# Kernel tuning notes

Measured on AMD Instinct MI355X. Metric: run time of the kernel, lower is better.

The kernel has to match this reference:

```python
import jax, jax.numpy as jnp
import numpy as np

N_HOPS = 2
N_ENTITIES = 100000
EMB = 64
N_REL = 32
N_EDGES = 1000000


def _l2norm(x, eps=1e-12):
    # torch F.normalize: x / max(||x||_2, eps) per row
    n = jnp.sqrt(jnp.sum(x * x, axis=1, keepdims=True))
    return x / jnp.maximum(n, eps)


def setup_inputs() -> dict:
    key = jax.random.key(0)
    k1, k2, k3, k4, k5, k6 = jax.random.split(key, 6)
    return {
        "entity_emb": jax.random.normal(k1, (N_ENTITIES, EMB), dtype=jnp.float32),
        "edge_emb": jax.random.normal(k2, (N_REL, EMB), dtype=jnp.float32) * 0.1,
        "q_w": jax.random.normal(k3, (EMB, EMB), dtype=jnp.float32) * (1.0 / np.sqrt(EMB)),
        "k_w": jax.random.normal(k4, (EMB, EMB), dtype=jnp.float32) * (1.0 / np.sqrt(EMB)),
        "edge_index": jax.random.randint(k5, (2, N_EDGES), 0, N_ENTITIES, dtype=jnp.int32),
        "edge_type": jax.random.randint(k6, (N_EDGES,), 0, N_REL, dtype=jnp.int32),
        "mess_dropout": 0,
    }


def reference(entity_emb, edge_emb, q_w, k_w, edge_index, edge_type, mess_dropout):
    head = edge_index[0]
    tail = edge_index[1]
    rel = edge_emb[edge_type]                      # [E, D]
    kg = jnp.zeros_like(entity_emb)
    agg = entity_emb
    for _ in range(N_HOPS):
        # edge-wise tanh attention score
        left = (agg @ q_w)[head]                   # [E, D] (factor GEMM out of gather)
        right = jnp.tanh((rel * agg[tail]) @ k_w)  # [E, D]
        att = jnp.sum(left * right, axis=1)        # [E]
        # scatter_softmax over head segments
        m = jax.ops.segment_max(att, head, num_segments=N_ENTITIES)
        e = jnp.exp(att - jax.lax.stop_gradient(m)[head])
        denom = jax.ops.segment_sum(e, head, num_segments=N_ENTITIES)
        w = e / denom[head]                        # [E]
        # weighted messages + scatter_mean aggregation
        msg = w[:, None] * rel * agg[tail]         # [E, D]
        s = jax.ops.segment_sum(msg, head, num_segments=N_ENTITIES)
        cnt = jax.ops.segment_sum(jnp.ones_like(w), head, num_segments=N_ENTITIES)
        agg = s / jnp.maximum(cnt, 1.0)[:, None]
        # mess_dropout=False path; normalize + residual accumulation
        agg = _l2norm(agg)
        kg = kg + agg + entity_emb
    return kg
```

## Files before the change

kernel.cpp:

```cpp
#include <hip/hip_runtime.h>
#include <math.h>

#define EMB 64
#define MAXREL 32
#define BSHIFT 9
#define BCAP 6912
#define CH 2048

typedef short bf16x8 __attribute__((ext_vector_type(8)));
typedef float f32x4 __attribute__((ext_vector_type(4)));

__device__ __forceinline__ short f2bf(float f) {
    unsigned u = __float_as_uint(f);
    u += 0x7FFFu + ((u >> 16) & 1u);
    return (short)(u >> 16);
}

#if __has_builtin(__builtin_amdgcn_cvt_pk_bf16_f32)
__device__ __forceinline__ short2 cvt2(float a, float b) {
    return __builtin_bit_cast(short2, __builtin_amdgcn_cvt_pk_bf16_f32(a, b));
}
#else
__device__ __forceinline__ short2 cvt2(float a, float b) {
    return make_short2(f2bf(a), f2bf(b));
}
#endif

__device__ __forceinline__ float lo_bf(unsigned d) { return __uint_as_float(d << 16); }
__device__ __forceinline__ float hi_bf(unsigned d) { return __uint_as_float(d & 0xffff0000u); }
__device__ __forceinline__ float bfs(short s) {
    return __uint_as_float(((unsigned)(unsigned short)s) << 16);
}

__device__ __forceinline__ bf16x8 pack8bf(uint4 U, float4 r0, float4 r1) {
    short2 c0 = cvt2(lo_bf(U.x) * r0.x, hi_bf(U.x) * r0.y);
    short2 c1 = cvt2(lo_bf(U.y) * r0.z, hi_bf(U.y) * r0.w);
    short2 c2 = cvt2(lo_bf(U.z) * r1.x, hi_bf(U.z) * r1.y);
    short2 c3 = cvt2(lo_bf(U.w) * r1.z, hi_bf(U.w) * r1.w);
    bf16x8 a;
    a[0] = c0.x; a[1] = c0.y; a[2] = c1.x; a[3] = c1.y;
    a[4] = c2.x; a[5] = c2.y; a[6] = c3.x; a[7] = c3.y;
    return a;
}

__device__ __forceinline__ float fast_rcp(float x) {
#if __has_builtin(__builtin_amdgcn_rcpf)
    return __builtin_amdgcn_rcpf(x);
#else
    return 1.0f / x;
#endif
}

__device__ __forceinline__ float fast_tanh(float x) {
    float ax = fabsf(x);
    float z = __expf(2.0f * ax);
    float r = 1.0f - 2.0f * fast_rcp(z + 1.0f);
    return copysignf(r, x);
}

__global__ void init_kernel(short4* __restrict__ aggbf, float4* __restrict__ kg,
                            const float4* __restrict__ ent, int n4) {
    int i = blockIdx.x * blockDim.x + threadIdx.x;
    if (i < n4) {
        float4 v = ent[i];
        short2 c0 = cvt2(v.x, v.y), c1 = cvt2(v.z, v.w);
        aggbf[i] = make_short4(c0.x, c0.y, c1.x, c1.y);
        kg[i] = make_float4(0.f, 0.f, 0.f, 0.f);
    }
}


__global__ void hist_kernel(int* __restrict__ deg, const int* __restrict__ head, int E) {
    int e = blockIdx.x * blockDim.x + threadIdx.x;
    if (e < E) atomicAdd(&deg[head[e]], 1);
}

__global__ void scan_blocks(const int* __restrict__ deg, int* __restrict__ excl,
                            int* __restrict__ bsum, int n) {
    __shared__ int wsum[4];
    int base = blockIdx.x * 1024;
    int t = threadIdx.x;
    int lane = t & 63, wid = t >> 6;
    int idx = base + t * 4;
    int v0 = (idx + 0 < n) ? deg[idx + 0] : 0;
    int v1 = (idx + 1 < n) ? deg[idx + 1] : 0;
    int v2 = (idx + 2 < n) ? deg[idx + 2] : 0;
    int v3 = (idx + 3 < n) ? deg[idx + 3] : 0;
    int s0 = v0, s1 = s0 + v1, s2 = s1 + v2, s3 = s2 + v3;
    int tsum = s3;
    int inc = tsum;
#pragma unroll
    for (int o = 1; o < 64; o <<= 1) { int u = __shfl_up(inc, o, 64); if (lane >= o) inc += u; }
    if (lane == 63) wsum[wid] = inc;
    __syncthreads();
    int woff = 0;
#pragma unroll
    for (int w = 0; w < 4; ++w) if (w < wid) woff += wsum[w];
    int texcl = woff + inc - tsum;
    if (idx + 0 < n) excl[idx + 0] = texcl;
    if (idx + 1 < n) excl[idx + 1] = texcl + s0;
    if (idx + 2 < n) excl[idx + 2] = texcl + s1;
    if (idx + 3 < n) excl[idx + 3] = texcl + s2;
    if (t == 255) bsum[blockIdx.x] = woff + inc;
}

__global__ void scan_sums(int* __restrict__ bsum, int* __restrict__ excl, int nb, int n, int E) {
    __shared__ int ws[4];
    int t = threadIdx.x;
    if (nb > 256) {
        if (t == 0) {
            int acc = 0;
            for (int b = 0; b < nb; ++b) { int v = bsum[b]; bsum[b] = acc; acc += v; }
            excl[n] = E;
        }
        return;
    }
    int lane = t & 63, wid = t >> 6;
    int v = (t < nb) ? bsum[t] : 0;
    int inc = v;
#pragma unroll
    for (int o = 1; o < 64; o <<= 1) { int u = __shfl_up(inc, o, 64); if (lane >= o) inc += u; }
    if (lane == 63) ws[wid] = inc;
    __syncthreads();
    int woff = 0;
#pragma unroll
    for (int w = 0; w < 4; ++w) if (w < wid) woff += ws[w];
    if (t < nb) bsum[t] = woff + inc - v;
    if (t == 0) excl[n] = E;
}

__global__ void scan_add(int* __restrict__ excl, const int* __restrict__ bsum, int n) {
    int i = blockIdx.x * blockDim.x + threadIdx.x;
    if (i < n) excl[i] += bsum[i >> 10];
}

__global__ void bucket_init(int* __restrict__ bcursor, const int* __restrict__ offsets,
                            int nb, int N) {
    int b = blockIdx.x * blockDim.x + threadIdx.x;
    if (b < nb) bcursor[b] = offsets[min(b << BSHIFT, N)];
}

__global__ void bucket_scatter(const int* __restrict__ head, const int* __restrict__ tail,
                               const int* __restrict__ etype, int* __restrict__ bcursor,
                               int2* __restrict__ tmp, int E, int nb) {
    __shared__ int lcnt[512];
    __shared__ int lbase[512];
    int t = threadIdx.x;
    int base = blockIdx.x * CH;
    for (int i = t; i < 512; i += 256) lcnt[i] = 0;
    __syncthreads();
    int myh[8];
#pragma unroll
    for (int i = 0; i < 8; ++i) {
        int e = base + i * 256 + t;
        if (e < E) {
            int h = head[e];
            myh[i] = h;
            atomicAdd(&lcnt[h >> BSHIFT], 1);
        } else myh[i] = -1;
    }
    __syncthreads();
    for (int b = t; b < nb; b += 256) {
        int c = lcnt[b];
        lbase[b] = (c > 0) ? atomicAdd(&bcursor[b], c) : 0;
        lcnt[b] = 0;
    }
    __syncthreads();
#pragma unroll
    for (int i = 0; i < 8; ++i) {
        int e = base + i * 256 + t;
        if (e < E) {
            int h = myh[i];
            int b = h >> BSHIFT;
            int pos = lbase[b] + atomicAdd(&lcnt[b], 1);
            tmp[pos] = make_int2(h, tail[e] | (etype[e] << 20));
        }
    }
}

__global__ void bucket_sort(const int* __restrict__ offsets, const int2* __restrict__ tmp,
                            int2* __restrict__ spair, int N) {
    __shared__ int2 staged[BCAP];
    __shared__ int lcur[1 << BSHIFT];
    int b = blockIdx.x;
    int h0 = b << BSHIFT;
    int h1 = min(h0 + (1 << BSHIFT), N);
    int r0 = offsets[h0], r1 = offsets[h1];
    int cnt = r1 - r0;
    int t = threadIdx.x;
    for (int h = h0 + t; h < h1; h += blockDim.x) lcur[h - h0] = offsets[h] - r0;
    __syncthreads();
    if (cnt <= BCAP) {
        for (int i = t; i < cnt; i += blockDim.x) {
            int2 rec = tmp[r0 + i];
            int lp = atomicAdd(&lcur[rec.x - h0], 1);
            staged[lp] = rec;
        }
        __syncthreads();
        for (int i = t; i < cnt; i += blockDim.x) spair[r0 + i] = staged[i];
    } else {
        for (int i = t; i < cnt; i += blockDim.x) {
            int2 rec = tmp[r0 + i];
            int lp = atomicAdd(&lcur[rec.x - h0], 1);
            spair[r0 + lp] = rec;
        }
    }
}


__device__ __forceinline__ void build_bfrags(bf16x8 bfrag[2][4], const float* __restrict__ W,
                                             int lane) {
    int koff = (lane >> 4) * 8;
    int n = lane & 15;
#pragma unroll
    for (int kh = 0; kh < 2; ++kh)
#pragma unroll
        for (int nt = 0; nt < 4; ++nt) {
            bf16x8 b;
#pragma unroll
            for (int j = 0; j < 8; ++j)
                b[j] = f2bf(W[(kh * 32 + koff + j) * EMB + nt * 16 + n]);
            bfrag[kh][nt] = b;
        }
}

__global__ void qproj_mfma_kernel(short* __restrict__ Qbf, const short* __restrict__ aggbf,
                                  const float* __restrict__ qw, int N) {
    int lane = threadIdx.x & 63;
    int gwave = blockIdx.x * (blockDim.x >> 6) + (threadIdx.x >> 6);
    int nwaves = gridDim.x * (blockDim.x >> 6);
    int row = lane & 15;
    int g = lane >> 4;
    int koff = g * 8;

    bf16x8 bfrag[2][4];
    build_bfrags(bfrag, qw, lane);

    int ntiles = (N + 15) >> 4;
    for (int tile = gwave; tile < ntiles; tile += nwaves) {
        int rIdx = min(tile * 16 + row, N - 1);
        const short* rowp = aggbf + (size_t)rIdx * EMB;
        bf16x8 a0 = *(const bf16x8*)(rowp + koff);
        bf16x8 a1 = *(const bf16x8*)(rowp + 32 + koff);
#pragma unroll
        for (int nt = 0; nt < 4; ++nt) {
            f32x4 acc = {0.f, 0.f, 0.f, 0.f};
            acc = __builtin_amdgcn_mfma_f32_16x16x32_bf16(a0, bfrag[0][nt], acc, 0, 0, 0);
            acc = __builtin_amdgcn_mfma_f32_16x16x32_bf16(a1, bfrag[1][nt], acc, 0, 0, 0);
#pragma unroll
            for (int reg = 0; reg < 4; ++reg) {
                int n2 = tile * 16 + g * 4 + reg;
                if (n2 < N) Qbf[(size_t)n2 * EMB + nt * 16 + (lane & 15)] = f2bf(acc[reg]);
            }
        }
    }
}

__global__ void att_mfma_kernel(float* __restrict__ att,
                                const short* __restrict__ aggbf, const short* __restrict__ Qbf,
                                const float* __restrict__ eemb, const float* __restrict__ kw,
                                const int2* __restrict__ spair, int E) {
    int lane = threadIdx.x & 63;
    int gwave = blockIdx.x * (blockDim.x >> 6) + (threadIdx.x >> 6);
    int nwaves = gridDim.x * (blockDim.x >> 6);
    int row = lane & 15;
    int g = lane >> 4;

    bf16x8 bfrag[2][4];
    build_bfrags(bfrag, kw, lane);

    int ntiles = (E + 15) >> 4;
    for (int tile = gwave; tile < ntiles; tile += nwaves) {
        int eld = min(tile * 16 + row, E - 1);
        int2 pr = spair[eld];
        int h = pr.x;
        int t = pr.y & 0xFFFFF;
        unsigned r = ((unsigned)pr.y) >> 20;
        const uint4* rowa = (const uint4*)(aggbf + (size_t)t * EMB);
        const float4* rl4 = (const float4*)(eemb + (size_t)r * EMB);
        uint4 U0 = rowa[g];
        uint4 U1 = rowa[4 + g];
        float4 y0 = rl4[g * 2], y1 = rl4[g * 2 + 1];
        float4 y2 = rl4[8 + g * 2], y3 = rl4[8 + g * 2 + 1];
        bf16x8 a0 = pack8bf(U0, y0, y1);
        bf16x8 a1 = pack8bf(U1, y2, y3);

        float sums0 = 0.f, sums1 = 0.f, sums2 = 0.f, sums3 = 0.f;
#pragma unroll
        for (int nt = 0; nt < 4; ++nt) {
            f32x4 acc = {0.f, 0.f, 0.f, 0.f};
            acc = __builtin_amdgcn_mfma_f32_16x16x32_bf16(a0, bfrag[0][nt], acc, 0, 0, 0);
            acc = __builtin_amdgcn_mfma_f32_16x16x32_bf16(a1, bfrag[1][nt], acc, 0, 0, 0);
#pragma unroll
            for (int reg = 0; reg < 4; ++reg) {
                int row2 = g * 4 + reg;
                int h2 = __shfl(h, row2, 64);
                float q = bfs(Qbf[(size_t)h2 * EMB + nt * 16 + (lane & 15)]);
                float v = q * fast_tanh(acc[reg]);
                if (reg == 0) sums0 += v;
                else if (reg == 1) sums1 += v;
                else if (reg == 2) sums2 += v;
                else sums3 += v;
            }
        }
#pragma unroll
        for (int m = 1; m <= 8; m <<= 1) {
            sums0 += __shfl_xor(sums0, m, 64);
            sums1 += __shfl_xor(sums1, m, 64);
            sums2 += __shfl_xor(sums2, m, 64);
            sums3 += __shfl_xor(sums3, m, 64);
        }
#pragma unroll
        for (int reg = 0; reg < 4; ++reg) {
            int row2 = g * 4 + reg;
            int e2 = tile * 16 + row2;
            float v = (reg == 0) ? sums0 : (reg == 1) ? sums1 : (reg == 2) ? sums2 : sums3;
            if ((lane & 15) == reg && e2 < E) att[e2] = v;
        }
    }
}

__global__ void head_agg_kernel(short* __restrict__ aggNewBf, float* __restrict__ kg,
                                const float* __restrict__ att, const short* __restrict__ aggOldBf,
                                const float* __restrict__ eemb, const float* __restrict__ ent,
                                const int* __restrict__ offsets, const int2* __restrict__ spair,
                                int N, int R) {
    __shared__ float4 elds4[MAXREL * 16];

    int tid = threadIdx.x;
    int lane = tid & 63;
    int wid = tid >> 6;
    int RS = (R < MAXREL) ? R : MAXREL;
    for (int i = tid; i < RS * 16; i += blockDim.x) elds4[i] = ((const float4*)eemb)[i];
    __syncthreads();

    int sub = lane >> 4;
    int q = lane & 15;
    int h = (blockIdx.x * (blockDim.x >> 6) + wid) * 4 + sub;
    if (h >= N) return;
    int beg = offsets[h], end = offsets[h + 1];
    int deg = end - beg;

    float m = -3.4e38f;
    for (int e = beg + q; e < end; e += 16) m = fmaxf(m, att[e]);
#pragma unroll
    for (int o = 1; o <= 8; o <<= 1) m = fmaxf(m, __shfl_xor(m, o, 64));

    float4 acc4 = make_float4(0.f, 0.f, 0.f, 0.f);
    float ssum = 0.f;
    int qbase = lane & 48;
    for (int c = beg; c < end; c += 16) {
        int e = c + q;
        float ev = 0.f; int tr = 0;
        if (e < end) {
            ev = __expf(att[e] - m);
            tr = spair[e].y;
        }
        ssum += ev;
        int nc = min(16, end - c);
        auto body = [&](int j) {
            int src = qbase | j;
            float ej = __shfl(ev, src, 64);
            int trj = __shfl(tr, src, 64);
            int tj = trj & 0xFFFFF;
            unsigned rj = ((unsigned)trj) >> 20;
            float4 ew = (rj < (unsigned)RS) ? elds4[rj * 16 + q]
                                            : ((const float4*)eemb)[(size_t)rj * 16 + q];
            uint2 X = ((const uint2*)(aggOldBf + (size_t)tj * EMB))[q];
            acc4.x += ej * ew.x * lo_bf(X.x);
            acc4.y += ej * ew.y * hi_bf(X.x);
            acc4.z += ej * ew.z * lo_bf(X.y);
            acc4.w += ej * ew.w * hi_bf(X.y);
        };
        if (nc == 16) {
#pragma unroll 4
            for (int j = 0; j < 16; ++j) body(j);
        } else {
            for (int j = 0; j < nc; ++j) body(j);
        }
    }
#pragma unroll
    for (int o = 1; o <= 8; o <<= 1) ssum += __shfl_xor(ssum, o, 64);

    float scale = (deg > 0) ? 1.0f / (ssum * (float)deg) : 0.f;
    float4 v = make_float4(acc4.x * scale, acc4.y * scale, acc4.z * scale, acc4.w * scale);
    float ss = v.x * v.x + v.y * v.y + v.z * v.z + v.w * v.w;
#pragma unroll
    for (int o = 1; o <= 8; o <<= 1) ss += __shfl_xor(ss, o, 64);
    float rinv = 1.0f / fmaxf(sqrtf(ss), 1e-12f);
    v.x *= rinv; v.y *= rinv; v.z *= rinv; v.w *= rinv;

    short2 c0 = cvt2(v.x, v.y), c1 = cvt2(v.z, v.w);
    ((short4*)aggNewBf)[(size_t)h * 16 + q] = make_short4(c0.x, c0.y, c1.x, c1.y);
    float4 kgv = ((float4*)kg)[(size_t)h * 16 + q];
    float4 ev2 = ((const float4*)ent)[(size_t)h * 16 + q];
    kgv.x += v.x + ev2.x; kgv.y += v.y + ev2.y;
    kgv.z += v.z + ev2.z; kgv.w += v.w + ev2.w;
    ((float4*)kg)[(size_t)h * 16 + q] = kgv;
}

extern "C" void kernel_launch(void* const* d_in, const int* in_sizes, int n_in,
                              void* d_out, int out_size, void* d_ws, size_t ws_size,
                              hipStream_t stream) {
    const float* ent  = (const float*)d_in[0];
    const float* eemb = (const float*)d_in[1];
    const float* qw   = (const float*)d_in[2];
    const float* kw   = (const float*)d_in[3];
    const int* eidx  = (const int*)d_in[4];
    const int* etype = (const int*)d_in[5];

    const int N = in_sizes[0] / EMB;
    const int R = in_sizes[1] / EMB;
    const int E = in_sizes[5];
    const int* head = eidx;
    const int* tail = eidx + E;

    float* kg = (float*)d_out;

    float* att   = (float*)d_ws;
    int2* spair  = (int2*)(att + E);
    int* offsets = (int*)(spair + E);
    int* deg     = offsets + (N + 1);
    int* bcursor = deg + N;
    int* bsum    = bcursor + N;
    uintptr_t pa = ((uintptr_t)(bsum + 1024) + 15) & ~(uintptr_t)15;
    short* aggbf_a = (short*)pa;
    short* aggbf_b = aggbf_a + (size_t)N * EMB;
    short* Qbf     = aggbf_b + (size_t)N * EMB;
    int2* tmp      = (int2*)Qbf;

    const int NT = 256;
    const int nb = (N + 1023) / 1024;
    const int nbk = (N + (1 << BSHIFT) - 1) >> BSHIFT;

    init_kernel<<<(N * EMB / 4 + NT - 1) / NT, NT, 0, stream>>>(
        (short4*)aggbf_a, (float4*)kg, (const float4*)ent, N * EMB / 4);
    hipMemsetAsync(deg, 0, (size_t)N * 4, stream);
    hist_kernel<<<(E + NT - 1) / NT, NT, 0, stream>>>(deg, head, E);
    scan_blocks<<<nb, NT, 0, stream>>>(deg, offsets, bsum, N);
    scan_sums<<<1, NT, 0, stream>>>(bsum, offsets, nb, N, E);
    scan_add<<<(N + NT - 1) / NT, NT, 0, stream>>>(offsets, bsum, N);
    bucket_init<<<(nbk + NT - 1) / NT, NT, 0, stream>>>(bcursor, offsets, nbk, N);
    bucket_scatter<<<(E + CH - 1) / CH, NT, 0, stream>>>(head, tail, etype, bcursor, tmp, E, nbk);
    bucket_sort<<<nbk, NT, 0, stream>>>(offsets, tmp, spair, N);

    short* curbf = aggbf_a;
    short* nxtbf = aggbf_b;
    for (int hop = 0; hop < 2; ++hop) {
        qproj_mfma_kernel<<<512, NT, 0, stream>>>(Qbf, curbf, qw, N);
        att_mfma_kernel<<<2048, NT, 0, stream>>>(att, curbf, Qbf, eemb, kw, spair, E);
        head_agg_kernel<<<(N + 15) / 16, NT, 0, stream>>>(nxtbf, kg, att, curbf,
                                                          eemb, ent, offsets, spair, N, R);
        short* ts = curbf; curbf = nxtbf; nxtbf = ts;
    }
}
```

Measured before the change: 420.0 us.

## Materialize per-edge rel*tail messages in att kernel and prefetch next tile

The attention kernel now writes each edge's bf16 rel*agg[tail] product (already computed as the MFMA A operand) to a workspace buffer in sorted-edge order. When the workspace is large enough, a new aggregation kernel reads those messages contiguously instead of gathering random tail rows and relation embeddings. The attention loop also software-prefetches the next tile's edge pair and tail rows and hoists the head-index shuffles. This trades 128 MB of extra writes and reads per hop for removing a random gather. The fallback path depends on workspace size, and the unroll factor is raised to 8.

```diff
diff --git a/kernel.cpp b/kernel.cpp
--- a/kernel.cpp
+++ b/kernel.cpp
@@ -42,6 +42,8 @@
     a[4] = c2.x; a[5] = c2.y; a[6] = c3.x; a[7] = c3.y;
     return a;
 }
+
+__device__ __forceinline__ uint4 asu4(bf16x8 v) { return __builtin_bit_cast(uint4, v); }
 
 __device__ __forceinline__ float fast_rcp(float x) {
 #if __has_builtin(__builtin_amdgcn_rcpf)
@@ -256,7 +258,7 @@
     }
 }
 
-__global__ void att_mfma_kernel(float* __restrict__ att,
+__global__ void att_mfma_kernel(float* __restrict__ att, short* __restrict__ Mout,
                                 const short* __restrict__ aggbf, const short* __restrict__ Qbf,
                                 const float* __restrict__ eemb, const float* __restrict__ kw,
                                 const int2* __restrict__ spair, int E) {
@@ -270,38 +272,63 @@
     build_bfrags(bfrag, kw, lane);
 
     int ntiles = (E + 15) >> 4;
-    for (int tile = gwave; tile < ntiles; tile += nwaves) {
-        int eld = min(tile * 16 + row, E - 1);
-        int2 pr = spair[eld];
+    int tile = gwave;
+    int2 pr = make_int2(0, 0);
+    uint4 U0 = make_uint4(0, 0, 0, 0), U1 = make_uint4(0, 0, 0, 0);
+    if (tile < ntiles) {
+        pr = spair[min(tile * 16 + row, E - 1)];
+        const uint4* rowa = (const uint4*)(aggbf + (size_t)(pr.y & 0xFFFFF) * EMB);
+        U0 = rowa[g];
+        U1 = rowa[4 + g];
+    }
+    for (; tile < ntiles; tile += nwaves) {
+        int tnext = tile + nwaves;
+        int2 prn = pr;
+        if (tnext < ntiles) prn = spair[min(tnext * 16 + row, E - 1)];
+
         int h = pr.x;
-        int t = pr.y & 0xFFFFF;
         unsigned r = ((unsigned)pr.y) >> 20;
-        const uint4* rowa = (const uint4*)(aggbf + (size_t)t * EMB);
         const float4* rl4 = (const float4*)(eemb + (size_t)r * EMB);
-        uint4 U0 = rowa[g];
-        uint4 U1 = rowa[4 + g];
         float4 y0 = rl4[g * 2], y1 = rl4[g * 2 + 1];
         float4 y2 = rl4[8 + g * 2], y3 = rl4[8 + g * 2 + 1];
         bf16x8 a0 = pack8bf(U0, y0, y1);
         bf16x8 a1 = pack8bf(U1, y2, y3);
 
+        uint4 U0n = U0, U1n = U1;
+        if (tnext < ntiles) {
+            const uint4* rowan = (const uint4*)(aggbf + (size_t)(prn.y & 0xFFFFF) * EMB);
+            U0n = rowan[g];
+            U1n = rowan[4 + g];
+        }
+
+        if (Mout) {
+            int e0 = tile * 16 + row;
+            if (e0 < E) {
+                uint4* mrow = (uint4*)(Mout + (size_t)e0 * EMB);
+                mrow[g] = asu4(a0);
+                mrow[4 + g] = asu4(a1);
+            }
+        }
+
+        int h2r0 = __shfl(h, g * 4 + 0, 64);
+        int h2r1 = __shfl(h, g * 4 + 1, 64);
+        int h2r2 = __shfl(h, g * 4 + 2, 64);
+        int h2r3 = __shfl(h, g * 4 + 3, 64);
+        const short* q0 = Qbf + (size_t)h2r0 * EMB + (lane & 15);
+        const short* q1 = Qbf + (size_t)h2r1 * EMB + (lane & 15);
+        const short* q2 = Qbf + (size_t)h2r2 * EMB + (lane & 15);
+        const short* q3 = Qbf + (size_t)h2r3 * EMB + (lane & 15);
+
         float sums0 = 0.f, sums1 = 0.f, sums2 = 0.f, sums3 = 0.f;
 #pragma unroll
         for (int nt = 0; nt < 4; ++nt) {
             f32x4 acc = {0.f, 0.f, 0.f, 0.f};
             acc = __builtin_amdgcn_mfma_f32_16x16x32_bf16(a0, bfrag[0][nt], acc, 0, 0, 0);
             acc = __builtin_amdgcn_mfma_f32_16x16x32_bf16(a1, bfrag[1][nt], acc, 0, 0, 0);
-#pragma unroll
-            for (int reg = 0; reg < 4; ++reg) {
-                int row2 = g * 4 + reg;
-                int h2 = __shfl(h, row2, 64);
-                float q = bfs(Qbf[(size_t)h2 * EMB + nt * 16 + (lane & 15)]);
-                float v = q * fast_tanh(acc[reg]);
-                if (reg == 0) sums0 += v;
-                else if (reg == 1) sums1 += v;
-                else if (reg == 2) sums2 += v;
-                else sums3 += v;
-            }
+            sums0 += bfs(q0[nt * 16]) * fast_tanh(acc[0]);
+            sums1 += bfs(q1[nt * 16]) * fast_tanh(acc[1]);
+            sums2 += bfs(q2[nt * 16]) * fast_tanh(acc[2]);
+            sums3 += bfs(q3[nt * 16]) * fast_tanh(acc[3]);
         }
 #pragma unroll
         for (int m = 1; m <= 8; m <<= 1) {
@@ -317,7 +344,71 @@
             float v = (reg == 0) ? sums0 : (reg == 1) ? sums1 : (reg == 2) ? sums2 : sums3;
             if ((lane & 15) == reg && e2 < E) att[e2] = v;
         }
-    }
+        pr = prn; U0 = U0n; U1 = U1n;
+    }
+}
+
+__global__ void head_agg_m_kernel(short* __restrict__ aggNewBf, float* __restrict__ kg,
+                                  const float* __restrict__ att, const short* __restrict__ M,
+                                  const float* __restrict__ ent, const int* __restrict__ offsets,
+                                  int N) {
+    int tid = threadIdx.x;
+    int lane = tid & 63;
+    int wid = tid >> 6;
+    int sub = lane >> 4;
+    int q = lane & 15;
+    int h = (blockIdx.x * (blockDim.x >> 6) + wid) * 4 + sub;
+    if (h >= N) return;
+    int beg = offsets[h], end = offsets[h + 1];
+    int deg = end - beg;
+
+    float m = -3.4e38f;
+    for (int e = beg + q; e < end; e += 16) m = fmaxf(m, att[e]);
+#pragma unroll
+    for (int o = 1; o <= 8; o <<= 1) m = fmaxf(m, __shfl_xor(m, o, 64));
+
+    float4 acc4 = make_float4(0.f, 0.f, 0.f, 0.f);
+    float ssum = 0.f;
+    int qbase = lane & 48;
+    for (int c = beg; c < end; c += 16) {
+        int e = c + q;
+        float ev = 0.f;
+        if (e < end) ev = __expf(att[e] - m);
+        ssum += ev;
+        int nc = min(16, end - c);
+        auto body = [&](int j) {
+            float ej = __shfl(ev, qbase | j, 64);
+            uint2 X = ((const uint2*)(M + (size_t)(c + j) * EMB))[q];
+            acc4.x += ej * lo_bf(X.x);
+            acc4.y += ej * hi_bf(X.x);
+            acc4.z += ej * lo_bf(X.y);
+            acc4.w += ej * hi_bf(X.y);
+        };
+        if (nc == 16) {
+#pragma unroll 8
+            for (int j = 0; j < 16; ++j) body(j);
+        } else {
+            for (int j = 0; j < nc; ++j) body(j);
+        }
+    }
+#pragma unroll
+    for (int o = 1; o <= 8; o <<= 1) ssum += __shfl_xor(ssum, o, 64);
+
+    float scale = (deg > 0) ? 1.0f / (ssum * (float)deg) : 0.f;
+    float4 v = make_float4(acc4.x * scale, acc4.y * scale, acc4.z * scale, acc4.w * scale);
+    float ss = v.x * v.x + v.y * v.y + v.z * v.z + v.w * v.w;
+#pragma unroll
+    for (int o = 1; o <= 8; o <<= 1) ss += __shfl_xor(ss, o, 64);
+    float rinv = 1.0f / fmaxf(sqrtf(ss), 1e-12f);
+    v.x *= rinv; v.y *= rinv; v.z *= rinv; v.w *= rinv;
+
+    short2 c0 = cvt2(v.x, v.y), c1 = cvt2(v.z, v.w);
+    ((short4*)aggNewBf)[(size_t)h * 16 + q] = make_short4(c0.x, c0.y, c1.x, c1.y);
+    float4 kgv = ((float4*)kg)[(size_t)h * 16 + q];
+    float4 ev2 = ((const float4*)ent)[(size_t)h * 16 + q];
+    kgv.x += v.x + ev2.x; kgv.y += v.y + ev2.y;
+    kgv.z += v.z + ev2.z; kgv.w += v.w + ev2.w;
+    ((float4*)kg)[(size_t)h * 16 + q] = kgv;
 }
 
 __global__ void head_agg_kernel(short* __restrict__ aggNewBf, float* __restrict__ kg,
@@ -373,7 +464,7 @@
             acc4.w += ej * ew.w * hi_bf(X.y);
         };
         if (nc == 16) {
-#pragma unroll 4
+#pragma unroll 8
             for (int j = 0; j < 16; ++j) body(j);
         } else {
             for (int j = 0; j < nc; ++j) body(j);
@@ -428,6 +519,9 @@
     short* aggbf_b = aggbf_a + (size_t)N * EMB;
     short* Qbf     = aggbf_b + (size_t)N * EMB;
     int2* tmp      = (int2*)Qbf;
+    short* M       = Qbf + (size_t)N * EMB;
+    size_t need_m  = (size_t)((char*)(M + (size_t)E * EMB) - (char*)d_ws);
+    bool useM = (ws_size >= need_m);
 
     const int NT = 256;
     const int nb = (N + 1023) / 1024;
@@ -448,9 +542,15 @@
     short* nxtbf = aggbf_b;
     for (int hop = 0; hop < 2; ++hop) {
         qproj_mfma_kernel<<<512, NT, 0, stream>>>(Qbf, curbf, qw, N);
-        att_mfma_kernel<<<2048, NT, 0, stream>>>(att, curbf, Qbf, eemb, kw, spair, E);
-        head_agg_kernel<<<(N + 15) / 16, NT, 0, stream>>>(nxtbf, kg, att, curbf,
-                                                          eemb, ent, offsets, spair, N, R);
+        att_mfma_kernel<<<2048, NT, 0, stream>>>(att, useM ? M : (short*)nullptr,
+                                                 curbf, Qbf, eemb, kw, spair, E);
+        if (useM) {
+            head_agg_m_kernel<<<(N + 15) / 16, NT, 0, stream>>>(nxtbf, kg, att, M, ent,
+                                                                offsets, N);
+        } else {
+            head_agg_kernel<<<(N + 15) / 16, NT, 0, stream>>>(nxtbf, kg, att, curbf,
+                                                              eemb, ent, offsets, spair, N, R);
+        }
         short* ts = curbf; curbf = nxtbf; nxtbf = ts;
     }
 }
```

New measurement: 427.6 us. About the same (+1.8%).

## Fuse attention scoring and head aggregation into one online-softmax kernel per head

Applied to the files above, without the earlier changes.

Replaces the separate edge-wise attention kernel and the per-head softmax/aggregation kernel with one kernel in which each wave processes one head's edges in chunks of 16. It computes MFMA scores, keeps a running max and sum, and rescales message accumulators online. This removes the att array round trip and the second gather of tail rows and relation embeddings. In exchange, each wave handles a single head, so low-degree heads leave most MFMA rows idle (about 10 edges per head on average). Messages are now built from bf16-rounded rel*agg products, which adds a small precision change.

```diff
diff --git a/kernel.cpp b/kernel.cpp
--- a/kernel.cpp
+++ b/kernel.cpp
@@ -256,147 +256,165 @@
     }
 }
 
-__global__ void att_mfma_kernel(float* __restrict__ att,
-                                const short* __restrict__ aggbf, const short* __restrict__ Qbf,
-                                const float* __restrict__ eemb, const float* __restrict__ kw,
-                                const int2* __restrict__ spair, int E) {
-    int lane = threadIdx.x & 63;
-    int gwave = blockIdx.x * (blockDim.x >> 6) + (threadIdx.x >> 6);
-    int nwaves = gridDim.x * (blockDim.x >> 6);
-    int row = lane & 15;
-    int g = lane >> 4;
+__global__ void fused_hop_kernel(short* __restrict__ aggNewBf, float* __restrict__ kg,
+                                 const short* __restrict__ aggOldBf,
+                                 const short* __restrict__ Qbf,
+                                 const float* __restrict__ eemb, const float* __restrict__ kw,
+                                 const float* __restrict__ ent,
+                                 const int* __restrict__ offsets,
+                                 const int2* __restrict__ spair, int N, int R) {
+    __shared__ float4 elds4[MAXREL * 16];
+
+    int tid = threadIdx.x;
+    int lane = tid & 63;
+    int RS = (R < MAXREL) ? R : MAXREL;
+    for (int i = tid; i < RS * 16; i += blockDim.x) elds4[i] = ((const float4*)eemb)[i];
 
     bf16x8 bfrag[2][4];
     build_bfrags(bfrag, kw, lane);
-
-    int ntiles = (E + 15) >> 4;
-    for (int tile = gwave; tile < ntiles; tile += nwaves) {
-        int eld = min(tile * 16 + row, E - 1);
-        int2 pr = spair[eld];
-        int h = pr.x;
-        int t = pr.y & 0xFFFFF;
-        unsigned r = ((unsigned)pr.y) >> 20;
-        const uint4* rowa = (const uint4*)(aggbf + (size_t)t * EMB);
-        const float4* rl4 = (const float4*)(eemb + (size_t)r * EMB);
-        uint4 U0 = rowa[g];
-        uint4 U1 = rowa[4 + g];
-        float4 y0 = rl4[g * 2], y1 = rl4[g * 2 + 1];
-        float4 y2 = rl4[8 + g * 2], y3 = rl4[8 + g * 2 + 1];
-        bf16x8 a0 = pack8bf(U0, y0, y1);
-        bf16x8 a1 = pack8bf(U1, y2, y3);
-
-        float sums0 = 0.f, sums1 = 0.f, sums2 = 0.f, sums3 = 0.f;
-#pragma unroll
-        for (int nt = 0; nt < 4; ++nt) {
-            f32x4 acc = {0.f, 0.f, 0.f, 0.f};
-            acc = __builtin_amdgcn_mfma_f32_16x16x32_bf16(a0, bfrag[0][nt], acc, 0, 0, 0);
-            acc = __builtin_amdgcn_mfma_f32_16x16x32_bf16(a1, bfrag[1][nt], acc, 0, 0, 0);
-#pragma unroll
-            for (int reg = 0; reg < 4; ++reg) {
-                int row2 = g * 4 + reg;
-                int h2 = __shfl(h, row2, 64);
-                float q = bfs(Qbf[(size_t)h2 * EMB + nt * 16 + (lane & 15)]);
-                float v = q * fast_tanh(acc[reg]);
-                if (reg == 0) sums0 += v;
-                else if (reg == 1) sums1 += v;
-                else if (reg == 2) sums2 += v;
-                else sums3 += v;
+    __syncthreads();
+
+    int g = lane >> 4;
+    int c = lane & 15;
+    int gwave = blockIdx.x * (blockDim.x >> 6) + (tid >> 6);
+    int nwaves = gridDim.x * (blockDim.x >> 6);
+
+    for (int h = gwave; h < N; h += nwaves) {
+        int beg = offsets[h], end = offsets[h + 1];
+        int deg = end - beg;
+
+        float accA[8], accB[8];
+#pragma unroll
+        for (int j = 0; j < 8; ++j) { accA[j] = 0.f; accB[j] = 0.f; }
+
+        if (deg > 0) {
+            const short* qrow = Qbf + (size_t)h * EMB;
+            float qv0 = bfs(qrow[0 + c]);
+            float qv1 = bfs(qrow[16 + c]);
+            float qv2 = bfs(qrow[32 + c]);
+            float qv3 = bfs(qrow[48 + c]);
+
+            float m_run = -3.4e38f, ssum = 0.f;
+
+            for (int cbeg = beg; cbeg < end; cbeg += 16) {
+                int ne = end - cbeg; if (ne > 16) ne = 16;
+                int2 rec = spair[min(cbeg + c, end - 1)];
+                int t = rec.y & 0xFFFFF;
+                unsigned r = ((unsigned)rec.y) >> 20;
+                const uint4* rowa = (const uint4*)(aggOldBf + (size_t)t * EMB);
+                uint4 U0 = rowa[g];
+                uint4 U1 = rowa[4 + g];
+                float4 y0, y1, y2, y3;
+                if (r < (unsigned)RS) {
+                    y0 = elds4[r * 16 + g * 2];     y1 = elds4[r * 16 + g * 2 + 1];
+                    y2 = elds4[r * 16 + 8 + g * 2]; y3 = elds4[r * 16 + 8 + g * 2 + 1];
+                } else {
+                    const float4* rl4 = (const float4*)(eemb + (size_t)r * EMB);
+                    y0 = rl4[g * 2]; y1 = rl4[g * 2 + 1];
+                    y2 = rl4[8 + g * 2]; y3 = rl4[8 + g * 2 + 1];
+                }
+                bf16x8 a0 = pack8bf(U0, y0, y1);
+                bf16x8 a1 = pack8bf(U1, y2, y3);
+
+                float attp[4] = {0.f, 0.f, 0.f, 0.f};
+#pragma unroll
+                for (int nt = 0; nt < 4; ++nt) {
+                    f32x4 acc = {0.f, 0.f, 0.f, 0.f};
+                    acc = __builtin_amdgcn_mfma_f32_16x16x32_bf16(a0, bfrag[0][nt], acc, 0, 0, 0);
+                    acc = __builtin_amdgcn_mfma_f32_16x16x32_bf16(a1, bfrag[1][nt], acc, 0, 0, 0);
+                    float qv = (nt == 0) ? qv0 : (nt == 1) ? qv1 : (nt == 2) ? qv2 : qv3;
+                    attp[0] += qv * fast_tanh(acc[0]);
+                    attp[1] += qv * fast_tanh(acc[1]);
+                    attp[2] += qv * fast_tanh(acc[2]);
+                    attp[3] += qv * fast_tanh(acc[3]);
+                }
+#pragma unroll
+                for (int reg = 0; reg < 4; ++reg) {
+#pragma unroll
+                    for (int o = 1; o <= 8; o <<= 1)
+                        attp[reg] += __shfl_xor(attp[reg], o, 64);
+                    attp[reg] = (g * 4 + reg < ne) ? attp[reg] : -3.4e38f;
+                }
+                float m4 = fmaxf(fmaxf(attp[0], attp[1]), fmaxf(attp[2], attp[3]));
+                m4 = fmaxf(m4, __shfl_xor(m4, 16, 64));
+                m4 = fmaxf(m4, __shfl_xor(m4, 32, 64));
+                float mnew = fmaxf(m_run, m4);
+                float scale = __expf(m_run - mnew);
+                float e0 = __expf(attp[0] - mnew), e1 = __expf(attp[1] - mnew);
+                float e2 = __expf(attp[2] - mnew), e3 = __expf(attp[3] - mnew);
+                float s4 = (e0 + e1) + (e2 + e3);
+                s4 += __shfl_xor(s4, 16, 64);
+                s4 += __shfl_xor(s4, 32, 64);
+                ssum = ssum * scale + s4;
+                int src = (c >> 2) << 4;
+                float t0 = __shfl(attp[0], src, 64);
+                float t1 = __shfl(attp[1], src, 64);
+                float t2 = __shfl(attp[2], src, 64);
+                float t3 = __shfl(attp[3], src, 64);
+                int cr = c & 3;
+                float av = (cr == 0) ? t0 : (cr == 1) ? t1 : (cr == 2) ? t2 : t3;
+                float w = __expf(av - mnew);
+                m_run = mnew;
+#pragma unroll
+                for (int j = 0; j < 8; ++j) {
+                    accA[j] = accA[j] * scale + w * bfs(a0[j]);
+                    accB[j] = accB[j] * scale + w * bfs(a1[j]);
+                }
             }
-        }
-#pragma unroll
-        for (int m = 1; m <= 8; m <<= 1) {
-            sums0 += __shfl_xor(sums0, m, 64);
-            sums1 += __shfl_xor(sums1, m, 64);
-            sums2 += __shfl_xor(sums2, m, 64);
-            sums3 += __shfl_xor(sums3, m, 64);
-        }
-#pragma unroll
-        for (int reg = 0; reg < 4; ++reg) {
-            int row2 = g * 4 + reg;
-            int e2 = tile * 16 + row2;
-            float v = (reg == 0) ? sums0 : (reg == 1) ? sums1 : (reg == 2) ? sums2 : sums3;
-            if ((lane & 15) == reg && e2 < E) att[e2] = v;
-        }
-    }
-}
-
-__global__ void head_agg_kernel(short* __restrict__ aggNewBf, float* __restrict__ kg,
-                                const float* __restrict__ att, const short* __restrict__ aggOldBf,
-                                const float* __restrict__ eemb, const float* __restrict__ ent,
-                                const int* __restrict__ offsets, const int2* __restrict__ spair,
-                                int N, int R) {
-    __shared__ float4 elds4[MAXREL * 16];
-
-    int tid = threadIdx.x;
-    int lane = tid & 63;
-    int wid = tid >> 6;
-    int RS = (R < MAXREL) ? R : MAXREL;
-    for (int i = tid; i < RS * 16; i += blockDim.x) elds4[i] = ((const float4*)eemb)[i];
-    __syncthreads();
-
-    int sub = lane >> 4;
-    int q = lane & 15;
-    int h = (blockIdx.x * (blockDim.x >> 6) + wid) * 4 + sub;
-    if (h >= N) return;
-    int beg = offsets[h], end = offsets[h + 1];
-    int deg = end - beg;
-
-    float m = -3.4e38f;
-    for (int e = beg + q; e < end; e += 16) m = fmaxf(m, att[e]);
-#pragma unroll
-    for (int o = 1; o <= 8; o <<= 1) m = fmaxf(m, __shfl_xor(m, o, 64));
-
-    float4 acc4 = make_float4(0.f, 0.f, 0.f, 0.f);
-    float ssum = 0.f;
-    int qbase = lane & 48;
-    for (int c = beg; c < end; c += 16) {
-        int e = c + q;
-        float ev = 0.f; int tr = 0;
-        if (e < end) {
-            ev = __expf(att[e] - m);
-            tr = spair[e].y;
-        }
-        ssum += ev;
-        int nc = min(16, end - c);
-        auto body = [&](int j) {
-            int src = qbase | j;
-            float ej = __shfl(ev, src, 64);
-            int trj = __shfl(tr, src, 64);
-            int tj = trj & 0xFFFFF;
-            unsigned rj = ((unsigned)trj) >> 20;
-            float4 ew = (rj < (unsigned)RS) ? elds4[rj * 16 + q]
-                                            : ((const float4*)eemb)[(size_t)rj * 16 + q];
-            uint2 X = ((const uint2*)(aggOldBf + (size_t)tj * EMB))[q];
-            acc4.x += ej * ew.x * lo_bf(X.x);
-            acc4.y += ej * ew.y * hi_bf(X.x);
-            acc4.z += ej * ew.z * lo_bf(X.y);
-            acc4.w += ej * ew.w * hi_bf(X.y);
-        };
-        if (nc == 16) {
-#pragma unroll 4
-            for (int j = 0; j < 16; ++j) body(j);
-        } else {
-            for (int j = 0; j < nc; ++j) body(j);
-        }
-    }
-#pragma unroll
-    for (int o = 1; o <= 8; o <<= 1) ssum += __shfl_xor(ssum, o, 64);
-
-    float scale = (deg > 0) ? 1.0f / (ssum * (float)deg) : 0.f;
-    float4 v = make_float4(acc4.x * scale, acc4.y * scale, acc4.z * scale, acc4.w * scale);
-    float ss = v.x * v.x + v.y * v.y + v.z * v.z + v.w * v.w;
-#pragma unroll
-    for (int o = 1; o <= 8; o <<= 1) ss += __shfl_xor(ss, o, 64);
-    float rinv = 1.0f / fmaxf(sqrtf(ss), 1e-12f);
-    v.x *= rinv; v.y *= rinv; v.z *= rinv; v.w *= rinv;
-
-    short2 c0 = cvt2(v.x, v.y), c1 = cvt2(v.z, v.w);
-    ((short4*)aggNewBf)[(size_t)h * 16 + q] = make_short4(c0.x, c0.y, c1.x, c1.y);
-    float4 kgv = ((float4*)kg)[(size_t)h * 16 + q];
-    float4 ev2 = ((const float4*)ent)[(size_t)h * 16 + q];
-    kgv.x += v.x + ev2.x; kgv.y += v.y + ev2.y;
-    kgv.z += v.z + ev2.z; kgv.w += v.w + ev2.w;
-    ((float4*)kg)[(size_t)h * 16 + q] = kgv;
+
+#pragma unroll
+            for (int j = 0; j < 8; ++j) {
+#pragma unroll
+                for (int o = 1; o <= 8; o <<= 1) {
+                    accA[j] += __shfl_xor(accA[j], o, 64);
+                    accB[j] += __shfl_xor(accB[j], o, 64);
+                }
+            }
+            float inv = fast_rcp(ssum * (float)deg);
+            float ss = 0.f;
+#pragma unroll
+            for (int j = 0; j < 8; ++j) {
+                accA[j] *= inv; accB[j] *= inv;
+                ss += accA[j] * accA[j] + accB[j] * accB[j];
+            }
+            ss += __shfl_xor(ss, 16, 64);
+            ss += __shfl_xor(ss, 32, 64);
+            float rinv = 1.0f / fmaxf(sqrtf(ss), 1e-12f);
+#pragma unroll
+            for (int j = 0; j < 8; ++j) { accA[j] *= rinv; accB[j] *= rinv; }
+        }
+
+        if (c == 0) {
+            short2 p0 = cvt2(accA[0], accA[1]), p1 = cvt2(accA[2], accA[3]);
+            short2 p2 = cvt2(accA[4], accA[5]), p3 = cvt2(accA[6], accA[7]);
+            short2 q0 = cvt2(accB[0], accB[1]), q1 = cvt2(accB[2], accB[3]);
+            short2 q2 = cvt2(accB[4], accB[5]), q3 = cvt2(accB[6], accB[7]);
+            uint4 WA = make_uint4(__builtin_bit_cast(unsigned, p0), __builtin_bit_cast(unsigned, p1),
+                                  __builtin_bit_cast(unsigned, p2), __builtin_bit_cast(unsigned, p3));
+            uint4 WB = make_uint4(__builtin_bit_cast(unsigned, q0), __builtin_bit_cast(unsigned, q1),
+                                  __builtin_bit_cast(unsigned, q2), __builtin_bit_cast(unsigned, q3));
+            uint4* arow = (uint4*)(aggNewBf + (size_t)h * EMB);
+            arow[g] = WA;
+            arow[4 + g] = WB;
+
+            float4* kg4 = (float4*)(kg + (size_t)h * EMB);
+            const float4* en4 = (const float4*)(ent + (size_t)h * EMB);
+            float4 ka0 = kg4[g * 2],     ka1 = kg4[g * 2 + 1];
+            float4 kb0 = kg4[8 + g * 2], kb1 = kg4[8 + g * 2 + 1];
+            float4 ea0 = en4[g * 2],     ea1 = en4[g * 2 + 1];
+            float4 eb0 = en4[8 + g * 2], eb1 = en4[8 + g * 2 + 1];
+            ka0.x += accA[0] + ea0.x; ka0.y += accA[1] + ea0.y;
+            ka0.z += accA[2] + ea0.z; ka0.w += accA[3] + ea0.w;
+            ka1.x += accA[4] + ea1.x; ka1.y += accA[5] + ea1.y;
+            ka1.z += accA[6] + ea1.z; ka1.w += accA[7] + ea1.w;
+            kb0.x += accB[0] + eb0.x; kb0.y += accB[1] + eb0.y;
+            kb0.z += accB[2] + eb0.z; kb0.w += accB[3] + eb0.w;
+            kb1.x += accB[4] + eb1.x; kb1.y += accB[5] + eb1.y;
+            kb1.z += accB[6] + eb1.z; kb1.w += accB[7] + eb1.w;
+            kg4[g * 2] = ka0;     kg4[g * 2 + 1] = ka1;
+            kg4[8 + g * 2] = kb0; kg4[8 + g * 2 + 1] = kb1;
+        }
+    }
 }
 
 extern "C" void kernel_launch(void* const* d_in, const int* in_sizes, int n_in,
@@ -448,9 +466,8 @@
     short* nxtbf = aggbf_b;
     for (int hop = 0; hop < 2; ++hop) {
         qproj_mfma_kernel<<<512, NT, 0, stream>>>(Qbf, curbf, qw, N);
-        att_mfma_kernel<<<2048, NT, 0, stream>>>(att, curbf, Qbf, eemb, kw, spair, E);
-        head_agg_kernel<<<(N + 15) / 16, NT, 0, stream>>>(nxtbf, kg, att, curbf,
-                                                          eemb, ent, offsets, spair, N, R);
+        fused_hop_kernel<<<4096, NT, 0, stream>>>(nxtbf, kg, curbf, Qbf, eemb, kw, ent,
+                                                  offsets, spair, N, R);
         short* ts = curbf; curbf = nxtbf; nxtbf = ts;
     }
 }
```

After: 540.7 us. 28.7% more time.
